# Kernel optimization log

Measured on AMD Instinct MI355X. Metric: run time of the kernel, lower is better.

## Reference

```python
import jax, jax.numpy as jnp
from jax import lax
import numpy as np

B, S, T, R = 64, 50, 50, 2   # batch, n_prev_sents, n_words, n_responses
V, H = 32000, 256            # vocab, hidden (= emb_size)


def gru_scan(xs, h0, Wih, Whh, bih, bhh):
    """Torch-style GRU over xs [T, N, I]; returns (outs [T,N,H], h_last [N,H])."""
    gi_all = jnp.einsum('tni,gi->tng', xs, Wih) + bih  # input gates precomputed
    def step(h, gi):
        gh = h @ Whh.T + bhh
        ir, iz, inn = jnp.split(gi, 3, -1)
        hr, hz, hn = jnp.split(gh, 3, -1)
        r = jax.nn.sigmoid(ir + hr)
        z = jax.nn.sigmoid(iz + hz)
        n = jnp.tanh(inn + r * hn)
        h = (1.0 - z) * n + z * h
        return h, h
    h_last, outs = lax.scan(step, h0, gi_all)
    return outs, h_last


def agent_tables():
    # replicates get_agent_emb: np.random.seed(1), one fresh uniform table per batch
    np.random.seed(1)
    return jnp.asarray(np.stack([np.random.uniform(0, 1, (S + 1, H)) for _ in range(B)]).astype(np.float32))


def setup_inputs() -> dict:
    key = jax.random.key(0)
    ks = jax.random.split(key, 24)
    k = 1.0 / np.sqrt(H)
    u = lambda kk, shape: jax.random.uniform(kk, shape, jnp.float32, -k, k)
    inp = {
        'context': jax.random.randint(ks[0], (B, S, T), 0, V, jnp.int32),
        'response': jax.random.randint(ks[1], (B, R, T), 0, V, jnp.int32),
        'spk_agents': jax.random.randint(ks[2], (B, S), 0, S + 1, jnp.int32),
        'emb_utter': jax.random.normal(ks[3], (V, H), jnp.float32) * 0.1,
        'emb_resp': jax.random.normal(ks[4], (V, H), jnp.float32) * 0.1,
        'utter_Wih': u(ks[5], (3 * H, H)), 'utter_Whh': u(ks[6], (3 * H, H)),
        'utter_bih': u(ks[7], (3 * H,)), 'utter_bhh': u(ks[8], (3 * H,)),
        'ctx_Wih': u(ks[9], (3 * H, 2 * H)), 'ctx_Whh': u(ks[10], (3 * H, H)),
        'ctx_bih': u(ks[11], (3 * H,)), 'ctx_bhh': u(ks[12], (3 * H,)),
        'resp_Wih': u(ks[13], (3 * H, H)), 'resp_Whh': u(ks[14], (3 * H, H)),
        'resp_bih': u(ks[15], (3 * H,)), 'resp_bhh': u(ks[16], (3 * H,)),
        'spk_Wih': u(ks[17], (3 * H, H)), 'spk_Whh': u(ks[18], (3 * H, H)),
        'spk_bih': u(ks[19], (3 * H,)), 'spk_bhh': u(ks[20], (3 * H,)),
    }
    return inp


def forward(context, response, spk_agents, emb_utter, emb_resp,
            utter_Wih, utter_Whh, utter_bih, utter_bhh,
            ctx_Wih, ctx_Whh, ctx_bih, ctx_bhh,
            resp_Wih, resp_Whh, resp_bih, resp_bhh,
            spk_Wih, spk_Whh, spk_bih, spk_bhh):
    # ---- utterance encoder: all B*S utterances batched through one GRU ----
    xu = emb_utter[context.reshape(B * S, T)]                 # [B*S, T, H]
    xu = jnp.transpose(xu, (1, 0, 2))                         # [T, B*S, H]
    _, hu = gru_scan(xu, jnp.zeros((B * S, H), jnp.float32),
                     utter_Wih, utter_Whh, utter_bih, utter_bhh)
    utter_hidden = hu.reshape(B, S, H).transpose(1, 0, 2)     # [S, B, H]

    # ---- agent embeddings (per-batch random tables, gathered by speaker id) ----
    tables = agent_tables()                                   # [B, S+1, H] constant
    agent_emb = jnp.take_along_axis(tables, spk_agents[:, :, None].astype(jnp.int32), axis=1)  # [B,S,H]
    agent_emb = jnp.transpose(agent_emb, (1, 0, 2))           # [S, B, H]

    # ---- context GRU over utterances ----
    ctx_in = jnp.concatenate([utter_hidden, agent_emb], axis=2)  # [S, B, 2H]
    context_output, ctx_h = gru_scan(ctx_in, jnp.zeros((B, H), jnp.float32),
                                     ctx_Wih, ctx_Whh, ctx_bih, ctx_bhh)
    context_hidden = ctx_h[None]                              # [1, B, H]

    # ---- speaker encoder: masked GRU == GRU over each speaker's subsequence ----
    sp_ids = jnp.arange(S + 1)
    active = (spk_agents[:, :, None] == sp_ids[None, None, :])  # [B, S, S+1]
    active_t = jnp.transpose(active, (1, 0, 2))                 # [S, B, S+1]
    gi_all = jnp.einsum('sbh,gh->sbg', context_output, spk_Wih) + spk_bih  # [S, B, 3H]

    def spk_step(h, inputs):
        gi, act = inputs                                        # gi [B,3H], act [B,S+1]
        gh = jnp.einsum('bsh,gh->bsg', h, spk_Whh) + spk_bhh    # [B, S+1, 3H]
        ir, iz, inn = jnp.split(gi[:, None, :], 3, -1)
        hr, hz, hn = jnp.split(gh, 3, -1)
        r = jax.nn.sigmoid(ir + hr)
        z = jax.nn.sigmoid(iz + hz)
        n = jnp.tanh(inn + r * hn)
        h_new = (1.0 - z) * n + z * h
        return jnp.where(act[:, :, None], h_new, h), None

    h_spk, _ = lax.scan(spk_step, jnp.zeros((B, S + 1, H), jnp.float32), (gi_all, active_t))
    present = active.any(axis=1)                               # [B, S+1]
    spk_emb = h_spk * present[:, :, None]                      # rows of absent speakers stay 0
    spk_emb_mask = (present & (sp_ids[None, :] > 0)).astype(jnp.float32)  # [B, S+1]

    # ---- response encoder: all B*R responses batched ----
    xr = emb_resp[response.reshape(B * R, T)]                  # [B*R, T, H]
    xr = jnp.transpose(xr, (1, 0, 2))                          # [T, B*R, H]
    outs, hr_ = gru_scan(xr, jnp.zeros((B * R, H), jnp.float32),
                         resp_Wih, resp_Whh, resp_bih, resp_bhh)
    resp_output = outs.reshape(T, B, R, H).transpose(2, 0, 1, 3)  # [R, T, B, H]
    resp_hidden = hr_.reshape(B, R, H).transpose(1, 0, 2)         # [R, B, H]

    return (context_output, context_hidden, resp_output, resp_hidden, spk_emb, spk_emb_mask)


def reference(context, response, spk_agents, emb_utter, emb_resp,
              utter_Wih, utter_Whh, utter_bih, utter_bhh,
              ctx_Wih, ctx_Whh, ctx_bih, ctx_bhh,
              resp_Wih, resp_Whh, resp_bih, resp_bhh,
              spk_Wih, spk_Whh, spk_bih, spk_bhh):
    return forward(context, response, spk_agents, emb_utter, emb_resp,
                   utter_Wih, utter_Whh, utter_bih, utter_bhh,
                   ctx_Wih, ctx_Whh, ctx_bih, ctx_bhh,
                   resp_Wih, resp_Whh, resp_bih, resp_bhh,
                   spk_Wih, spk_Whh, spk_bih, spk_bhh)
```

## Files before the change

kernel.cpp:

```cpp
#include <hip/hip_runtime.h>
#include <hip/hip_bf16.h>
#include <stdint.h>
#include <stdlib.h>
#include <math.h>

typedef __hip_bfloat16 bf16;
typedef unsigned short ushort;
typedef __attribute__((ext_vector_type(8))) short bhalf8;
typedef __attribute__((ext_vector_type(4))) float f32x4;

#define Bn 64
#define Sn 50
#define Tn 50
#define Hn 256

#define OFF_CTX_OUT   0
#define OFF_CTX_HID   819200
#define OFF_RESP_OUT  835584
#define OFF_RESP_HID  2473984
#define OFF_SPK_EMB   2506752
#define OFF_SPK_MASK  3342336

#define WS_FLAG   0u
#define WS_HU     256u
#define WS_REG    1638912u
#define RG_UTTQ   0u
#define RG_UTTSC  24576000u
#define RG_RESPGI 0u
#define RG_CO     9830400u
#define RG_GIC    13107200u
#define RG_GIS    18022400u
#define RG_TBL    22937600u
#define WS_END    26342912u

__device__ __forceinline__ float b2f_bits(unsigned int b) {
    union { unsigned int u; float f; } c; c.u = b; return c.f;
}
__device__ __forceinline__ float bf2f(ushort v) { return b2f_bits(((unsigned int)v) << 16); }
__device__ __forceinline__ ushort f2bf(float f) {
    union { float f; unsigned int u; } c; c.f = f;
    return (ushort)((c.u + 0x7fffu + ((c.u >> 16) & 1u)) >> 16);
}
__device__ __forceinline__ void gld_lds16(const void* g, void* l) {
    __builtin_amdgcn_global_load_lds(
        (const __attribute__((address_space(1))) void*)g,
        (__attribute__((address_space(3))) void*)l, 16, 0, 0);
}
template<bool BF>
__device__ __forceinline__ bhalf8 ldfrag(const void* __restrict__ p, size_t i) {
    if (BF) {
        return *(const bhalf8*)((const ushort*)p + i);
    } else {
        const float* q = (const float*)p + i;
        float4 a = *(const float4*)q;
        float4 b = *(const float4*)(q + 4);
        bhalf8 r;
        r[0] = (short)f2bf(a.x); r[1] = (short)f2bf(a.y);
        r[2] = (short)f2bf(a.z); r[3] = (short)f2bf(a.w);
        r[4] = (short)f2bf(b.x); r[5] = (short)f2bf(b.y);
        r[6] = (short)f2bf(b.z); r[7] = (short)f2bf(b.w);
        return r;
    }
}
template<bool BF>
__device__ __forceinline__ float ldw(const void* __restrict__ p, int i) {
    return BF ? bf2f(((const ushort*)p)[i]) : ((const float*)p)[i];
}
template<bool BF>
__device__ __forceinline__ void stout(void* __restrict__ out, size_t i, float v) {
    if (BF) ((ushort*)out)[i] = f2bf(v);
    else    ((float*)out)[i] = v;
}
__device__ __forceinline__ float fsigm(float x) {
    return __builtin_amdgcn_rcpf(1.f + __expf(-x));
}
__device__ __forceinline__ float ftanh(float x) {
    float e = __expf(-2.f * x);
    return (1.f - e) * __builtin_amdgcn_rcpf(1.f + e);
}

__global__ void sniff_kernel(const void* __restrict__ w, int* __restrict__ flag) {
    const unsigned int* p = (const unsigned int*)w;
    int tid = threadIdx.x;
    bool big = false;
// ... 230 lines not shown
    const int* __restrict__ rsp_tok, const void* __restrict__ emb_r,
    const void* __restrict__ rWih, const void* __restrict__ rbih,
    ushort* __restrict__ RG, float* bhs)
{
    const int tid = threadIdx.x;
    const int w = tid >> 6, l = tid & 63, quad = l >> 4, c = l & 15;

    for (int i = tid; i < 768; i += 512) bhs[i] = ldw<BF>(rbih, i);

    bhalf8 wf[3][2][8];
    #pragma unroll
    for (int g = 0; g < 3; ++g)
        #pragma unroll
        for (int ctl = 0; ctl < 2; ++ctl) {
            const int gcol = g * 256 + 32 * w + 16 * ctl + c;
            #pragma unroll
            for (int tk = 0; tk < 8; ++tk)
                wf[g][ctl][tk] = ldfrag<BF>(rWih, (size_t)gcol * 256 + 32 * tk + 8 * quad);
        }
    __syncthreads();

    const int inst = bid * 16 + c;
    const int tok  = rsp_tok[inst];

    f32x4 acc[3][2];
    #pragma unroll
    for (int g = 0; g < 3; ++g)
        #pragma unroll
        for (int ctl = 0; ctl < 2; ++ctl) {
            float b = bhs[g * 256 + 32 * w + 16 * ctl + c];
            acc[g][ctl] = (f32x4){b, b, b, b};
        }
    #pragma unroll
    for (int tk = 0; tk < 8; ++tk) {
        bhalf8 a = ldfrag<BF>(emb_r, (size_t)tok * 256 + 32 * tk + 8 * quad);
        #pragma unroll
        for (int g = 0; g < 3; ++g)
            #pragma unroll
            for (int ctl = 0; ctl < 2; ++ctl)
                acc[g][ctl] = __builtin_amdgcn_mfma_f32_16x16x32_bf16(
                    a, wf[g][ctl][tk], acc[g][ctl], 0, 0, 0);
    }
    #pragma unroll
    for (int g = 0; g < 3; ++g)
        #pragma unroll
        for (int ctl = 0; ctl < 2; ++ctl)
            #pragma unroll
            for (int r = 0; r < 4; ++r)
                RG[(size_t)(bid * 16 + 4 * quad + r) * 768
                   + g * 256 + 32 * w + 16 * ctl + c] = f2bf(acc[g][ctl][r]);
}

template<bool BF>
__device__ void rec_resp_body(
    int bid,
    const ushort* __restrict__ RG,
    const void* __restrict__ rWhh, const void* __restrict__ rbhh,
    void* __restrict__ outp,
    ushort (*gx)[16][776], ushort (*hb)[16][264])
{
    const int n0 = bid * 16;
    const int tid = threadIdx.x;
    const int w = tid >> 6, l = tid & 63, quad = l >> 4, c = l & 15;

    for (int i = tid; i < 16 * 264; i += 512) (&hb[0][0][0])[i] = 0;

    float breg[3][2];
    #pragma unroll
    for (int g = 0; g < 3; ++g)
        #pragma unroll
        for (int ctl = 0; ctl < 2; ++ctl)
            breg[g][ctl] = ldw<BF>(rbhh, g * 256 + 32 * w + 16 * ctl + c);

    bhalf8 wf[3][2][8];
    #pragma unroll
    for (int g = 0; g < 3; ++g)
        #pragma unroll
        for (int ctl = 0; ctl < 2; ++ctl) {
            const int gcol = g * 256 + 32 * w + 16 * ctl + c;
            #pragma unroll
            for (int tk = 0; tk < 8; ++tk)
                wf[g][ctl][tk] = ldfrag<BF>(rWhh, (size_t)gcol * 256 + 32 * tk + 8 * quad);
        }

    float st[2][4];
    #pragma unroll
    for (int ctl = 0; ctl < 2; ++ctl)
        #pragma unroll
        for (int r = 0; r < 4; ++r) st[ctl][r] = 0.f;

    #pragma unroll
    for (int k = 0; k < 2; ++k) {
        const int m = 2 * w + k;
        const ushort* src = RG + (size_t)((n0 + m) * Tn + 0) * 768;
        if (l < 48) {
            gld_lds16(src + l * 8,       &gx[0][m][0]);
            gld_lds16(src + 384 + l * 8, &gx[0][m][384]);
        }
    }
    __syncthreads();

    int p = 0;
    for (int t = 0; t < Tn; ++t) {
        if (t < Tn - 1) {
            #pragma unroll
            for (int k = 0; k < 2; ++k) {
                const int m = 2 * w + k;
                const ushort* src = RG + (size_t)((n0 + m) * Tn + t + 1) * 768;
                if (l < 48) {
                    gld_lds16(src + l * 8,       &gx[p ^ 1][m][0]);
                    gld_lds16(src + 384 + l * 8, &gx[p ^ 1][m][384]);
                }
            }
// ... 15 lines not shown
        f32x4 acc[3][2];
        #pragma unroll
        for (int g = 0; g < 3; ++g)
            #pragma unroll
            for (int ctl = 0; ctl < 2; ++ctl) {
                float b = breg[g][ctl];
                acc[g][ctl] = (f32x4){b, b, b, b};
            }
        #pragma unroll
        for (int tk = 0; tk < 8; ++tk) {
            bhalf8 a = *(const bhalf8*)(&hb[p][c][32 * tk + 8 * quad]);
            #pragma unroll
            for (int g = 0; g < 3; ++g)
                #pragma unroll
                for (int ctl = 0; ctl < 2; ++ctl)
                    acc[g][ctl] = __builtin_amdgcn_mfma_f32_16x16x32_bf16(
                        a, wf[g][ctl][tk], acc[g][ctl], 0, 0, 0);
        }

        #pragma unroll
        for (int ctl = 0; ctl < 2; ++ctl) {
            const int u = 32 * w + 16 * ctl + c;
            #pragma unroll
            for (int r = 0; r < 4; ++r) {
                const int m = 4 * quad + r;
                float gr = bf2f(gx[p][m][u]);
                float gz = bf2f(gx[p][m][256 + u]);
                float gn = bf2f(gx[p][m][512 + u]);
                float rr = fsigm(gr + acc[0][ctl][r]);
                float zz = fsigm(gz + acc[1][ctl][r]);
                float nn = ftanh(gn + rr * acc[2][ctl][r]);
                float h  = (1.f - zz) * nn + zz * st[ctl][r];
                st[ctl][r] = h;
                hb[p ^ 1][m][u] = f2bf(h);
            }
        }
        __syncthreads();
        p ^= 1;
    }

    #pragma unroll
    for (int ctl = 0; ctl < 2; ++ctl) {
        const int u = 32 * w + 16 * ctl + c;
        #pragma unroll
        for (int r = 0; r < 4; ++r) {
            const int n = n0 + 4 * quad + r, bb = n >> 1, ri = n & 1;
            stout<BF>(outp, OFF_RESP_OUT
                      + (size_t)((ri * Tn + (Tn - 1)) * Bn + bb) * Hn + u, st[ctl][r]);
            stout<BF>(outp, OFF_RESP_HID + (size_t)(ri * Bn + bb) * Hn + u, st[ctl][r]);
        }
    }
}

template<bool BF>
__device__ void gi_ctx_body(
    int bid,
    const ushort* __restrict__ H_u, const ushort* __restrict__ tblbf,
    const int* __restrict__ spk_agents,
    const void* __restrict__ Wih, const void* __restrict__ bih,
    ushort* __restrict__ GIc, float* bhs)
{
    const int tid = threadIdx.x;
    const int w = tid >> 6, l = tid & 63, quad = l >> 4, c = l & 15;

    for (int i = tid; i < 768; i += 512) bhs[i] = ldw<BF>(bih, i);
    __syncthreads();

    const int m0 = bid * 16;
    const int m  = m0 + c, s = m >> 6, b = m & 63;
    const int a  = spk_agents[b * Sn + s];
    const ushort* arow0 = H_u   + (size_t)(b * Sn + s) * Hn;
    const ushort* arow1 = tblbf + (size_t)(b * 51 + a) * Hn;

    f32x4 acc[3][2];
    #pragma unroll
    for (int g = 0; g < 3; ++g)
        #pragma unroll
        for (int ctl = 0; ctl < 2; ++ctl) {
            float bb = bhs[g * 256 + 32 * w + 16 * ctl + c];
            acc[g][ctl] = (f32x4){bb, bb, bb, bb};
        }

    for (int half = 0; half < 2; ++half) {
        const ushort* ar = half ? arow1 : arow0;
        bhalf8 af[8];
        #pragma unroll
        for (int tk = 0; tk < 8; ++tk)
            af[tk] = *(const bhalf8*)(ar + 32 * tk + 8 * quad);
        #pragma unroll
        for (int g = 0; g < 3; ++g) {
            bhalf8 wf[2][8];
            #pragma unroll
            for (int ctl = 0; ctl < 2; ++ctl) {
                const int gcol = g * 256 + 32 * w + 16 * ctl + c;
                #pragma unroll
                for (int tk = 0; tk < 8; ++tk)
                    wf[ctl][tk] = ldfrag<BF>(Wih,
                        (size_t)gcol * 512 + half * 256 + 32 * tk + 8 * quad);
            }
            #pragma unroll
            for (int tk = 0; tk < 8; ++tk)
                #pragma unroll
                for (int ctl = 0; ctl < 2; ++ctl)
                    acc[g][ctl] = __builtin_amdgcn_mfma_f32_16x16x32_bf16(
                        af[tk], wf[ctl][tk], acc[g][ctl], 0, 0, 0);
        }
    }

    #pragma unroll
    for (int g = 0; g < 3; ++g)
        #pragma unroll
        for (int ctl = 0; ctl < 2; ++ctl)
            #pragma unroll
            for (int r = 0; r < 4; ++r)
                GIc[(size_t)(m0 + 4 * quad + r) * 768
                    + g * 256 + 32 * w + 16 * ctl + c] = f2bf(acc[g][ctl][r]);
}

__global__ __launch_bounds__(512, 1) void gates2_kernel(
    const int* rsp_tok, const void* emb_r, const void* rWih, const void* rbih,
    ushort* RG,
    const ushort* H_u, const ushort* tblbf, const int* spk_agents,
    const void* cWih, const void* cbih, ushort* GIc, const int* flag)
{
    __shared__ float bhs[768];
    if (blockIdx.x < 400) {
        if (*flag) respgi_body<true >(blockIdx.x, rsp_tok, emb_r, rWih, rbih, RG, bhs);
        else       respgi_body<false>(blockIdx.x, rsp_tok, emb_r, rWih, rbih, RG, bhs);
    } else {
        const int bid = blockIdx.x - 400;
        if (*flag) gi_ctx_body<true >(bid, H_u, tblbf, spk_agents, cWih, cbih, GIc, bhs);
        else       gi_ctx_body<false>(bid, H_u, tblbf, spk_agents, cWih, cbih, GIc, bhs);
    }
}

template<bool BF>
__device__ void ctx_rec_body(
    int bid,
    const ushort* __restrict__ GIc,
    const void* __restrict__ Whh, const void* __restrict__ bhh,
    float* __restrict__ CO, void* __restrict__ outp,
    ushort (*gx)[16][776], ushort (*hb)[16][264])
{
    const int n0 = bid * 16;
    const int tid = threadIdx.x;
    const int w = tid >> 6, l = tid & 63, quad = l >> 4, c = l & 15;

    for (int i = tid; i < 16 * 264; i += 512) (&hb[0][0][0])[i] = 0;

    float breg[3][2];
    #pragma unroll
    for (int g = 0; g < 3; ++g)
        #pragma unroll
        for (int ctl = 0; ctl < 2; ++ctl)
            breg[g][ctl] = ldw<BF>(bhh, g * 256 + 32 * w + 16 * ctl + c);

    bhalf8 wf[3][2][8];
    #pragma unroll
    for (int g = 0; g < 3; ++g)
        #pragma unroll
        for (int ctl = 0; ctl < 2; ++ctl) {
            const int gcol = g * 256 + 32 * w + 16 * ctl + c;
            #pragma unroll
            for (int tk = 0; tk < 8; ++tk)
                wf[g][ctl][tk] = ldfrag<BF>(Whh, (size_t)gcol * 256 + 32 * tk + 8 * quad);
        }

    float st[2][4];
    #pragma unroll
    for (int ctl = 0; ctl < 2; ++ctl)
        #pragma unroll
        for (int r = 0; r < 4; ++r) st[ctl][r] = 0.f;

    #pragma unroll
    for (int k = 0; k < 2; ++k) {
        const int m = 2 * w + k;
        const ushort* src = GIc + (size_t)(0 * Bn + n0 + m) * 768;
        if (l < 48) {
            gld_lds16(src + l * 8,       &gx[0][m][0]);
            gld_lds16(src + 384 + l * 8, &gx[0][m][384]);
        }
    }
    __syncthreads();

    int p = 0;
    for (int t = 0; t < Sn; ++t) {
        if (t < Sn - 1) {
            #pragma unroll
            for (int k = 0; k < 2; ++k) {
                const int m = 2 * w + k;
                const ushort* src = GIc + (size_t)((t + 1) * Bn + n0 + m) * 768;
                if (l < 48) {
                    gld_lds16(src + l * 8,       &gx[p ^ 1][m][0]);
                    gld_lds16(src + 384 + l * 8, &gx[p ^ 1][m][384]);
                }
            }
        }
        if (t > 0) {
            #pragma unroll
            for (int ctl = 0; ctl < 2; ++ctl) {
                const int u = 32 * w + 16 * ctl + c;
                #pragma unroll
                for (int r = 0; r < 4; ++r) {
                    const size_t gri = (size_t)((t - 1) * Bn + n0 + 4 * quad + r);
                    CO[gri * Hn + u] = st[ctl][r];
                    stout<BF>(outp, OFF_CTX_OUT + gri * Hn + u, st[ctl][r]);
                }
            }
        }

        f32x4 acc[3][2];
        #pragma unroll
        for (int g = 0; g < 3; ++g)
            #pragma unroll
            for (int ctl = 0; ctl < 2; ++ctl) {
                float b = breg[g][ctl];
                acc[g][ctl] = (f32x4){b, b, b, b};
            }
        #pragma unroll
        for (int tk = 0; tk < 8; ++tk) {
            bhalf8 a = *(const bhalf8*)(&hb[p][c][32 * tk + 8 * quad]);
            #pragma unroll
            for (int g = 0; g < 3; ++g)
                #pragma unroll
                for (int ctl = 0; ctl < 2; ++ctl)
                    acc[g][ctl] = __builtin_amdgcn_mfma_f32_16x16x32_bf16(
                        a, wf[g][ctl][tk], acc[g][ctl], 0, 0, 0);
        }

        #pragma unroll
        for (int ctl = 0; ctl < 2; ++ctl) {
            const int u = 32 * w + 16 * ctl + c;
            #pragma unroll
            for (int r = 0; r < 4; ++r) {
                const int m = 4 * quad + r;
                float gr = bf2f(gx[p][m][u]);
                float gz = bf2f(gx[p][m][256 + u]);
                float gn = bf2f(gx[p][m][512 + u]);
                float rr = fsigm(gr + acc[0][ctl][r]);
                float zz = fsigm(gz + acc[1][ctl][r]);
                float nn = ftanh(gn + rr * acc[2][ctl][r]);
                float h  = (1.f - zz) * nn + zz * st[ctl][r];
                st[ctl][r] = h;
                hb[p ^ 1][m][u] = f2bf(h);
            }
        }
        __syncthreads();
        p ^= 1;
    }

    #pragma unroll
    for (int ctl = 0; ctl < 2; ++ctl) {
        const int u = 32 * w + 16 * ctl + c;
        #pragma unroll
        for (int r = 0; r < 4; ++r) {
            const int m = 4 * quad + r;
            const size_t gri = (size_t)((Sn - 1) * Bn + n0 + m);
            CO[gri * Hn + u] = st[ctl][r];
            stout<BF>(outp, OFF_CTX_OUT + gri * Hn + u, st[ctl][r]);
            stout<BF>(outp, OFF_CTX_HID + (size_t)(n0 + m) * Hn + u, st[ctl][r]);
        }
    }
}

__global__ __launch_bounds__(512, 1) void rec2_kernel(
    const ushort* GIc, const void* cWhh, const void* cbhh, float* CO,
    const ushort* RG, const void* rWhh, const void* rbhh,
    void* outp, const int* flag)
{
    __shared__ __align__(16) ushort gx[2][16][776];
    __shared__ __align__(16) ushort hb[2][16][264];
    if (blockIdx.x < 4) {
        if (*flag) ctx_rec_body<true >(blockIdx.x, GIc, cWhh, cbhh, CO, outp, gx, hb);
        else       ctx_rec_body<false>(blockIdx.x, GIc, cWhh, cbhh, CO, outp, gx, hb);
    } else {
        const int bid = blockIdx.x - 4;
        if (*flag) rec_resp_body<true >(bid, RG, rWhh, rbhh, outp, gx, hb);
        else       rec_resp_body<false>(bid, RG, rWhh, rbhh, outp, gx, hb);
    }
}

template<bool BF>
__device__ void gi_spk_body(
    const float* __restrict__ CO,
    const void* __restrict__ Wih, const void* __restrict__ bih,
    ushort* __restrict__ GIs, float* bhs)
{
    const int tid = threadIdx.x;
    const int w = tid >> 6, l = tid & 63, quad = l >> 4, c = l & 15;

    for (int i = tid; i < 768; i += 512) bhs[i] = ldw<BF>(bih, i);

    bhalf8 wf[3][2][8];
    #pragma unroll
    for (int g = 0; g < 3; ++g)
        #pragma unroll
        for (int ctl = 0; ctl < 2; ++ctl) {
            const int gcol = g * 256 + 32 * w + 16 * ctl + c;
            #pragma unroll
            for (int tk = 0; tk < 8; ++tk)
                wf[g][ctl][tk] = ldfrag<BF>(Wih, (size_t)gcol * 256 + 32 * tk + 8 * quad);
        }
    __syncthreads();

    f32x4 acc[3][2];
    #pragma unroll
    for (int g = 0; g < 3; ++g)
        #pragma unroll
        for (int ctl = 0; ctl < 2; ++ctl) {
            float b = bhs[g * 256 + 32 * w + 16 * ctl + c];
            acc[g][ctl] = (f32x4){b, b, b, b};
        }
    #pragma unroll
    for (int tk = 0; tk < 8; ++tk) {
        bhalf8 a = ldfrag<false>(CO, (size_t)(blockIdx.x * 16 + c) * 256 + 32 * tk + 8 * quad);
        #pragma unroll
        for (int g = 0; g < 3; ++g)
            #pragma unroll
            for (int ctl = 0; ctl < 2; ++ctl)
                acc[g][ctl] = __builtin_amdgcn_mfma_f32_16x16x32_bf16(
                    a, wf[g][ctl][tk], acc[g][ctl], 0, 0, 0);
    }
    #pragma unroll
    for (int g = 0; g < 3; ++g)
        #pragma unroll
        for (int ctl = 0; ctl < 2; ++ctl)
            #pragma unroll
            for (int r = 0; r < 4; ++r)
                GIs[(size_t)(blockIdx.x * 16 + 4 * quad + r) * 768
                    + g * 256 + 32 * w + 16 * ctl + c] = f2bf(acc[g][ctl][r]);
}

__global__ __launch_bounds__(512, 1) void gi_spk_kernel(
    const float* CO, const void* Wih, const void* bih, ushort* GIs, const int* flag)
{
    __shared__ float bhs[768];
    if (*flag) gi_spk_body<true >(CO, Wih, bih, GIs, bhs);
    else       gi_spk_body<false>(CO, Wih, bih, GIs, bhs);
}

#define SSTR 264
template<bool BF>
__device__ void spk_rec_body(
    const ushort* __restrict__ GIs,
    const void* __restrict__ Whh, const void* __restrict__ bhh,
    const int* __restrict__ spk_agents,
    void* __restrict__ outp,
    ushort* S , ushort (*gx)[4][776], int* pres , float* bhs)
{
    const int b0 = blockIdx.x * 4;
    const int tid = threadIdx.x;
    const int w = tid >> 6, l = tid & 63, quad = l >> 4, c = l & 15;

    for (int i = tid; i < 768; i += 512) bhs[i] = ldw<BF>(bhh, i);
    for (int i = tid; i < 4 * 51 * SSTR; i += 512) S[i] = 0;
    for (int i = tid; i < 4 * 51; i += 512) pres[i] = 0;

    bhalf8 wf[3][2][8];
    #pragma unroll
    for (int g = 0; g < 3; ++g)
        #pragma unroll
        for (int ctl = 0; ctl < 2; ++ctl) {
            const int gcol = g * 256 + 32 * w + 16 * ctl + c;
            #pragma unroll
            for (int tk = 0; tk < 8; ++tk)
                wf[g][ctl][tk] = ldfrag<BF>(Whh, (size_t)gcol * 256 + 32 * tk + 8 * quad);
        }

    {
        const int row = w >> 1, ch = w & 1;
        const ushort* src = GIs + (size_t)(0 * Bn + b0 + row) * 768 + ch * 384;
        if (l < 48) gld_lds16(src + l * 8, &gx[0][row][ch * 384]);
    }
    __syncthreads();

    int p = 0;
    for (int t = 0; t < Sn; ++t) {
        const int va = (c < 4) ? spk_agents[(b0 + c) * Sn + t] : 0;
        const int mb = (c < 4) ? c : 0;

        if (t < Sn - 1) {
            const int row = w >> 1, ch = w & 1;
            const ushort* src = GIs + (size_t)((t + 1) * Bn + b0 + row) * 768 + ch * 384;
            if (l < 48) gld_lds16(src + l * 8, &gx[p ^ 1][row][ch * 384]);
        }

        f32x4 acc[3][2];
        #pragma unroll
        for (int g = 0; g < 3; ++g)
            #pragma unroll
            for (int ctl = 0; ctl < 2; ++ctl) {
                float b = bhs[g * 256 + 32 * w + 16 * ctl + c];
                acc[g][ctl] = (f32x4){b, b, b, b};
            }
        const ushort* srow = &S[(mb * 51 + va) * SSTR];
        #pragma unroll
        for (int tk = 0; tk < 8; ++tk) {
            bhalf8 a = *(const bhalf8*)(srow + 32 * tk + 8 * quad);
            #pragma unroll
            for (int g = 0; g < 3; ++g)
                #pragma unroll
                for (int ctl = 0; ctl < 2; ++ctl)
                    acc[g][ctl] = __builtin_amdgcn_mfma_f32_16x16x32_bf16(
                        a, wf[g][ctl][tk], acc[g][ctl], 0, 0, 0);
        }
        __syncthreads();

        if (quad == 0) {
            int vv[4];
            #pragma unroll
            for (int r = 0; r < 4; ++r) vv[r] = spk_agents[(b0 + r) * Sn + t];
            #pragma unroll
            for (int ctl = 0; ctl < 2; ++ctl) {
                const int u = 32 * w + 16 * ctl + c;
                #pragma unroll
                for (int r = 0; r < 4; ++r) {
                    ushort* sp = &S[(r * 51 + vv[r]) * SSTR + u];
                    float gr = bf2f(gx[p][r][u]);
                    float gz = bf2f(gx[p][r][256 + u]);
                    float gn = bf2f(gx[p][r][512 + u]);
                    float hprev = bf2f(*sp);
                    float rr = fsigm(gr + acc[0][ctl][r]);
                    float zz = fsigm(gz + acc[1][ctl][r]);
                    float nn = ftanh(gn + rr * acc[2][ctl][r]);
                    float h  = (1.f - zz) * nn + zz * hprev;
                    *sp = f2bf(h);
                }
            }
        }
        if (tid < 4) pres[tid * 51 + spk_agents[(b0 + tid) * Sn + t]] = 1;
        __syncthreads();
        p ^= 1;
    }
    __syncthreads();

    for (int idx = tid; idx < 4 * 51 * 256; idx += 512) {
        const int mb2 = idx / (51 * 256);
        const int rem = idx - mb2 * (51 * 256);
        const int v = rem >> 8, u = rem & 255;
        float val = bf2f(S[(mb2 * 51 + v) * SSTR + u]);
        stout<BF>(outp, OFF_SPK_EMB + (size_t)((b0 + mb2) * 51 + v) * Hn + u, val);
    }
    for (int idx = tid; idx < 4 * 51; idx += 512) {
        const int mb2 = idx / 51, v = idx - mb2 * 51;
        stout<BF>(outp, OFF_SPK_MASK + (size_t)((b0 + mb2) * 51 + v),
                  (pres[mb2 * 51 + v] && v > 0) ? 1.f : 0.f);
    }
}

__global__ __launch_bounds__(512, 1) void spk_rec_kernel(
    const ushort* GIs, const void* Whh, const void* bhh,
    const int* spk_agents, void* outp, const int* flag)
{
    __shared__ __align__(16) ushort S[4 * 51 * SSTR];
    __shared__ __align__(16) ushort gx[2][4][776];
    __shared__ int    pres[4 * 51];
    __shared__ float  bhs[768];
    if (*flag) spk_rec_body<true >(GIs, Whh, bhh, spk_agents, outp, S, gx, pres, bhs);
    else       spk_rec_body<false>(GIs, Whh, bhh, spk_agents, outp, S, gx, pres, bhs);
}

namespace {
inline uint16_t host_f2bf(float f) {
    union { float f; uint32_t u; } c; c.f = f;
    return (uint16_t)((c.u + 0x7fffu + ((c.u >> 16) & 1u)) >> 16);
}
struct MT19937 {
    uint32_t mt[624]; int mti;
    void seed(uint32_t s) {
        mt[0] = s;
        for (int i = 1; i < 624; ++i)
            mt[i] = 1812433253u * (mt[i - 1] ^ (mt[i - 1] >> 30)) + (uint32_t)i;
        mti = 624;
    }
    uint32_t next() {
        if (mti >= 624) {
            for (int i = 0; i < 624; ++i) {
                uint32_t y = (mt[i] & 0x80000000u) | (mt[(i + 1) % 624] & 0x7fffffffu);
                mt[i] = mt[(i + 397) % 624] ^ (y >> 1) ^ ((y & 1u) ? 0x9908b0dfu : 0u);
            }
            mti = 0;
        }
        uint32_t y = mt[mti++];
        y ^= y >> 11; y ^= (y << 7) & 0x9d2c5680u; y ^= (y << 15) & 0xefc60000u; y ^= y >> 18;
        return y;
    }
    double rd() {
        uint32_t a = next() >> 5, b = next() >> 6;
        return (a * 67108864.0 + b) / 9007199254740992.0;
    }
};

uint16_t* get_host_tables() {
    static uint16_t* p = [] {
        void* q = nullptr;
        if (hipHostMalloc(&q, 835584 * sizeof(uint16_t), hipHostMallocDefault) != hipSuccess)
            q = malloc(835584 * sizeof(uint16_t));
        uint16_t* h = (uint16_t*)q;
        MT19937 g; g.seed(1u);
        for (int i = 0; i < 835584; ++i)
            h[i] = host_f2bf((float)g.rd());
        return h;
    }();
    return p;
}
}

extern "C" void kernel_launch(void* const* d_in, const int* in_sizes, int n_in,
                              void* d_out, int out_size, void* d_ws, size_t ws_size,
                              hipStream_t stream)
{
    const int* ctx_tok    = (const int*)d_in[0];
    const int* rsp_tok    = (const int*)d_in[1];
    const int* spk_agents = (const int*)d_in[2];
    const void* emb_u = d_in[3];
    const void* emb_r = d_in[4];
    const void* uWih = d_in[5],  *uWhh = d_in[6],  *ubih = d_in[7],  *ubhh = d_in[8];
    const void* cWih = d_in[9],  *cWhh = d_in[10], *cbih = d_in[11], *cbhh = d_in[12];
    const void* rWih = d_in[13], *rWhh = d_in[14], *rbih = d_in[15], *rbhh = d_in[16];
    const void* sWih = d_in[17], *sWhh = d_in[18], *sbih = d_in[19], *sbhh = d_in[20];
    (void)in_sizes; (void)n_in; (void)out_size; (void)ws_size;

    char* ws  = (char*)d_ws;
    char* reg = ws + WS_REG;
    int*      flag = (int*)(ws + WS_FLAG);
    ushort*   H_u  = (ushort*)(ws + WS_HU);
    char*     UQ   = (char*)(reg + RG_UTTQ);
    float*    USC  = (float*)(reg + RG_UTTSC);
    ushort*   RG   = (ushort*)(reg + RG_RESPGI);
    float*    CO   = (float*)(reg + RG_CO);
    ushort*   GIc  = (ushort*)(reg + RG_GIC);
    ushort*   GIs  = (ushort*)(reg + RG_GIS);
    ushort*   tbl  = (ushort*)(reg + RG_TBL);
    void*     out  = d_out;

    sniff_kernel<<<1, 64, 0, stream>>>(uWih, flag);

    vocab_utt_kernel<<<250, 512, 0, stream>>>(emb_u, uWih, ubih, UQ, USC, flag);
    rec_utt_kernel<<<200, 512, 0, stream>>>(ctx_tok, UQ, USC, uWhh, ubhh, H_u, flag);

    hipMemcpyAsync(tbl, get_host_tables(), 835584 * sizeof(uint16_t),
                   hipMemcpyHostToDevice, stream);

    gates2_kernel<<<600, 512, 0, stream>>>(rsp_tok, emb_r, rWih, rbih, RG,
                                           H_u, tbl, spk_agents, cWih, cbih, GIc, flag);

    rec2_kernel<<<12, 512, 0, stream>>>(GIc, cWhh, cbhh, CO,
                                        RG, rWhh, rbhh, out, flag);

    gi_spk_kernel<<<200, 512, 0, stream>>>(CO, sWih, sbih, GIs, flag);
    spk_rec_kernel<<<16, 512, 0, stream>>>(GIs, sWhh, sbhh, spk_agents, out, flag);
}
```

Before: 1.236 ms.

## Fuse context GRU recurrence, speaker input gates and speaker recurrence into one kernel

Replaces the context recurrence, the speaker input-gate GEMM and the speaker recurrence kernels with a single kernel. Each block now handles 4 batches through the context GRU and feeds each step's hidden state directly into the speaker GRU, computing the speaker input gates per step instead of precomputing them. This removes two launches, the CO and GIs global round trips and a grid-wide dependency. In exchange, weights are reloaded from global/cache every step rather than held in registers, context parallelism falls to 16 blocks of 4 rows, and the speaker work is now serialized behind the context recurrence inside each block.

```diff
diff --git a/kernel.cpp b/kernel.cpp
--- a/kernel.cpp
+++ b/kernel.cpp
@@ -27,9 +27,7 @@
 #define RG_UTTQ   0u
 #define RG_UTTSC  24576000u
 #define RG_RESPGI 0u
-#define RG_CO     9830400u
 #define RG_GIC    13107200u
-#define RG_GIS    18022400u
 #define RG_TBL    22937600u
 #define WS_END    26342912u
 
@@ -366,13 +364,97 @@
 }
 
 template<bool BF>
+__device__ void gi_ctx_body(
+    int bid,
+    const ushort* __restrict__ H_u, const ushort* __restrict__ tblbf,
+    const int* __restrict__ spk_agents,
+    const void* __restrict__ Wih, const void* __restrict__ bih,
+    ushort* __restrict__ GIc, float* bhs)
+{
+    const int tid = threadIdx.x;
+    const int w = tid >> 6, l = tid & 63, quad = l >> 4, c = l & 15;
+
+    for (int i = tid; i < 768; i += 512) bhs[i] = ldw<BF>(bih, i);
+    __syncthreads();
+
+    const int m0 = bid * 16;
+    const int m  = m0 + c, s = m >> 6, b = m & 63;
+    const int a  = spk_agents[b * Sn + s];
+    const ushort* arow0 = H_u   + (size_t)(b * Sn + s) * Hn;
+    const ushort* arow1 = tblbf + (size_t)(b * 51 + a) * Hn;
+
+    f32x4 acc[3][2];
+    #pragma unroll
+    for (int g = 0; g < 3; ++g)
+        #pragma unroll
+        for (int ctl = 0; ctl < 2; ++ctl) {
+            float bb = bhs[g * 256 + 32 * w + 16 * ctl + c];
+            acc[g][ctl] = (f32x4){bb, bb, bb, bb};
+        }
+
+    for (int half = 0; half < 2; ++half) {
+        const ushort* ar = half ? arow1 : arow0;
+        bhalf8 af[8];
+        #pragma unroll
+        for (int tk = 0; tk < 8; ++tk)
+            af[tk] = *(const bhalf8*)(ar + 32 * tk + 8 * quad);
+        #pragma unroll
+        for (int g = 0; g < 3; ++g) {
+            bhalf8 wfl[2][8];
+            #pragma unroll
+            for (int ctl = 0; ctl < 2; ++ctl) {
+                const int gcol = g * 256 + 32 * w + 16 * ctl + c;
+                #pragma unroll
+                for (int tk = 0; tk < 8; ++tk)
+                    wfl[ctl][tk] = ldfrag<BF>(Wih,
+                        (size_t)gcol * 512 + half * 256 + 32 * tk + 8 * quad);
+            }
+            #pragma unroll
+            for (int tk = 0; tk < 8; ++tk)
+                #pragma unroll
+                for (int ctl = 0; ctl < 2; ++ctl)
+                    acc[g][ctl] = __builtin_amdgcn_mfma_f32_16x16x32_bf16(
+                        af[tk], wfl[ctl][tk], acc[g][ctl], 0, 0, 0);
+        }
+    }
+
+    #pragma unroll
+    for (int g = 0; g < 3; ++g)
+        #pragma unroll
+        for (int ctl = 0; ctl < 2; ++ctl)
+            #pragma unroll
+            for (int r = 0; r < 4; ++r)
+                GIc[(size_t)(m0 + 4 * quad + r) * 768
+                    + g * 256 + 32 * w + 16 * ctl + c] = f2bf(acc[g][ctl][r]);
+}
+
+__global__ __launch_bounds__(512, 1) void gates2_kernel(
+    const int* rsp_tok, const void* emb_r, const void* rWih, const void* rbih,
+    ushort* RG,
+    const ushort* H_u, const ushort* tblbf, const int* spk_agents,
+    const void* cWih, const void* cbih, ushort* GIc, const int* flag)
+{
+    __shared__ float bhs[768];
+    if (blockIdx.x < 400) {
+        if (*flag) respgi_body<true >(blockIdx.x, rsp_tok, emb_r, rWih, rbih, RG, bhs);
+        else       respgi_body<false>(blockIdx.x, rsp_tok, emb_r, rWih, rbih, RG, bhs);
+    } else {
+        const int bid = blockIdx.x - 400;
+        if (*flag) gi_ctx_body<true >(bid, H_u, tblbf, spk_agents, cWih, cbih, GIc, bhs);
+        else       gi_ctx_body<false>(bid, H_u, tblbf, spk_agents, cWih, cbih, GIc, bhs);
+    }
+}
+
+template<bool BF>
 __device__ void rec_resp_body(
     int bid,
     const ushort* __restrict__ RG,
     const void* __restrict__ rWhh, const void* __restrict__ rbhh,
-    void* __restrict__ outp,
-    ushort (*gx)[16][776], ushort (*hb)[16][264])
-{
+    void* __restrict__ outp, char* smem)
+{
+    ushort (*gx)[16][776] = (ushort(*)[16][776])(smem);
+    ushort (*hb)[16][264] = (ushort(*)[16][264])(smem + 49664);
+
     const int n0 = bid * 16;
     const int tid = threadIdx.x;
     const int w = tid >> 6, l = tid & 63, quad = l >> 4, c = l & 15;
@@ -494,119 +576,37 @@
     }
 }
 
+#define SSTR 264
 template<bool BF>
-__device__ void gi_ctx_body(
+__device__ void mega_body(
     int bid,
-    const ushort* __restrict__ H_u, const ushort* __restrict__ tblbf,
+    const ushort* __restrict__ GIc,
+    const void* __restrict__ cWhh, const void* __restrict__ cbhh,
+    const void* __restrict__ sWih, const void* __restrict__ sbih,
+    const void* __restrict__ sWhh, const void* __restrict__ sbhh,
     const int* __restrict__ spk_agents,
-    const void* __restrict__ Wih, const void* __restrict__ bih,
-    ushort* __restrict__ GIc, float* bhs)
-{
+    void* __restrict__ outp, char* smem)
+{
+    ushort* S             = (ushort*)smem;
+    ushort (*hc)[16][264] = (ushort(*)[16][264])(smem + 107712);
+    ushort (*gic)[4][776] = (ushort(*)[4][776])(smem + 124608);
+    int*    pres          = (int*)(smem + 137024);
+    float*  cbh           = (float*)(smem + 137840);
+    float*  sbi           = cbh + 768;
+    float*  sbh           = sbi + 768;
+
+    const int b0 = bid * 4;
     const int tid = threadIdx.x;
     const int w = tid >> 6, l = tid & 63, quad = l >> 4, c = l & 15;
 
-    for (int i = tid; i < 768; i += 512) bhs[i] = ldw<BF>(bih, i);
-    __syncthreads();
-
-    const int m0 = bid * 16;
-    const int m  = m0 + c, s = m >> 6, b = m & 63;
-    const int a  = spk_agents[b * Sn + s];
-    const ushort* arow0 = H_u   + (size_t)(b * Sn + s) * Hn;
-    const ushort* arow1 = tblbf + (size_t)(b * 51 + a) * Hn;
-
-    f32x4 acc[3][2];
-    #pragma unroll
-    for (int g = 0; g < 3; ++g)
-        #pragma unroll
-        for (int ctl = 0; ctl < 2; ++ctl) {
-            float bb = bhs[g * 256 + 32 * w + 16 * ctl + c];
-            acc[g][ctl] = (f32x4){bb, bb, bb, bb};
-        }
-
-    for (int half = 0; half < 2; ++half) {
-        const ushort* ar = half ? arow1 : arow0;
-        bhalf8 af[8];
-        #pragma unroll
-        for (int tk = 0; tk < 8; ++tk)
-            af[tk] = *(const bhalf8*)(ar + 32 * tk + 8 * quad);
-        #pragma unroll
-        for (int g = 0; g < 3; ++g) {
-            bhalf8 wf[2][8];
-            #pragma unroll
-            for (int ctl = 0; ctl < 2; ++ctl) {
-                const int gcol = g * 256 + 32 * w + 16 * ctl + c;
-                #pragma unroll
-                for (int tk = 0; tk < 8; ++tk)
-                    wf[ctl][tk] = ldfrag<BF>(Wih,
-                        (size_t)gcol * 512 + half * 256 + 32 * tk + 8 * quad);
-            }
-            #pragma unroll
-            for (int tk = 0; tk < 8; ++tk)
-                #pragma unroll
-                for (int ctl = 0; ctl < 2; ++ctl)
-                    acc[g][ctl] = __builtin_amdgcn_mfma_f32_16x16x32_bf16(
-                        af[tk], wf[ctl][tk], acc[g][ctl], 0, 0, 0);
-        }
-    }
-
-    #pragma unroll
-    for (int g = 0; g < 3; ++g)
-        #pragma unroll
-        for (int ctl = 0; ctl < 2; ++ctl)
-            #pragma unroll
-            for (int r = 0; r < 4; ++r)
-                GIc[(size_t)(m0 + 4 * quad + r) * 768
-                    + g * 256 + 32 * w + 16 * ctl + c] = f2bf(acc[g][ctl][r]);
-}
-
-__global__ __launch_bounds__(512, 1) void gates2_kernel(
-    const int* rsp_tok, const void* emb_r, const void* rWih, const void* rbih,
-    ushort* RG,
-    const ushort* H_u, const ushort* tblbf, const int* spk_agents,
-    const void* cWih, const void* cbih, ushort* GIc, const int* flag)
-{
-    __shared__ float bhs[768];
-    if (blockIdx.x < 400) {
-        if (*flag) respgi_body<true >(blockIdx.x, rsp_tok, emb_r, rWih, rbih, RG, bhs);
-        else       respgi_body<false>(blockIdx.x, rsp_tok, emb_r, rWih, rbih, RG, bhs);
-    } else {
-        const int bid = blockIdx.x - 400;
-        if (*flag) gi_ctx_body<true >(bid, H_u, tblbf, spk_agents, cWih, cbih, GIc, bhs);
-        else       gi_ctx_body<false>(bid, H_u, tblbf, spk_agents, cWih, cbih, GIc, bhs);
-    }
-}
-
-template<bool BF>
-__device__ void ctx_rec_body(
-    int bid,
-    const ushort* __restrict__ GIc,
-    const void* __restrict__ Whh, const void* __restrict__ bhh,
-    float* __restrict__ CO, void* __restrict__ outp,
-    ushort (*gx)[16][776], ushort (*hb)[16][264])
-{
-    const int n0 = bid * 16;
-    const int tid = threadIdx.x;
-    const int w = tid >> 6, l = tid & 63, quad = l >> 4, c = l & 15;
-
-    for (int i = tid; i < 16 * 264; i += 512) (&hb[0][0][0])[i] = 0;
-
-    float breg[3][2];
-    #pragma unroll
-    for (int g = 0; g < 3; ++g)
-        #pragma unroll
-        for (int ctl = 0; ctl < 2; ++ctl)
-            breg[g][ctl] = ldw<BF>(bhh, g * 256 + 32 * w + 16 * ctl + c);
-
-    bhalf8 wf[3][2][8];
-    #pragma unroll
-    for (int g = 0; g < 3; ++g)
-        #pragma unroll
-        for (int ctl = 0; ctl < 2; ++ctl) {
-            const int gcol = g * 256 + 32 * w + 16 * ctl + c;
-            #pragma unroll
-            for (int tk = 0; tk < 8; ++tk)
-                wf[g][ctl][tk] = ldfrag<BF>(Whh, (size_t)gcol * 256 + 32 * tk + 8 * quad);
-        }
+    for (int i = tid; i < 4 * 51 * SSTR; i += 512) S[i] = 0;
+    for (int i = tid; i < 2 * 16 * 264; i += 512) (&hc[0][0][0])[i] = 0;
+    for (int i = tid; i < 4 * 51; i += 512) pres[i] = 0;
+    for (int i = tid; i < 768; i += 512) {
+        cbh[i] = ldw<BF>(cbhh, i);
+        sbi[i] = ldw<BF>(sbih, i);
+        sbh[i] = ldw<BF>(sbhh, i);
+    }
 
     float st[2][4];
     #pragma unroll
@@ -614,238 +614,125 @@
         #pragma unroll
         for (int r = 0; r < 4; ++r) st[ctl][r] = 0.f;
 
-    #pragma unroll
-    for (int k = 0; k < 2; ++k) {
-        const int m = 2 * w + k;
-        const ushort* src = GIc + (size_t)(0 * Bn + n0 + m) * 768;
-        if (l < 48) {
-            gld_lds16(src + l * 8,       &gx[0][m][0]);
-            gld_lds16(src + 384 + l * 8, &gx[0][m][384]);
-        }
+    {
+        const int row = w >> 1, ch = w & 1;
+        const ushort* src = GIc + (size_t)(0 * Bn + b0 + row) * 768 + ch * 384;
+        if (l < 48) gld_lds16(src + l * 8, &gic[0][row][ch * 384]);
     }
     __syncthreads();
 
     int p = 0;
     for (int t = 0; t < Sn; ++t) {
         if (t < Sn - 1) {
-            #pragma unroll
-            for (int k = 0; k < 2; ++k) {
-                const int m = 2 * w + k;
-                const ushort* src = GIc + (size_t)((t + 1) * Bn + n0 + m) * 768;
-                if (l < 48) {
-                    gld_lds16(src + l * 8,       &gx[p ^ 1][m][0]);
-                    gld_lds16(src + 384 + l * 8, &gx[p ^ 1][m][384]);
+            const int row = w >> 1, ch = w & 1;
+            const ushort* src = GIc + (size_t)((t + 1) * Bn + b0 + row) * 768 + ch * 384;
+            if (l < 48) gld_lds16(src + l * 8, &gic[p ^ 1][row][ch * 384]);
+        }
+
+        bhalf8 areg[8];
+        #pragma unroll
+        for (int tk = 0; tk < 8; ++tk)
+            areg[tk] = *(const bhalf8*)(&hc[p][c][32 * tk + 8 * quad]);
+        f32x4 accc[3][2];
+        #pragma unroll
+        for (int g = 0; g < 3; ++g)
+            #pragma unroll
+            for (int ctl = 0; ctl < 2; ++ctl) {
+                float b = cbh[g * 256 + 32 * w + 16 * ctl + c];
+                accc[g][ctl] = (f32x4){b, b, b, b};
+            }
+        #pragma unroll
+        for (int g = 0; g < 3; ++g)
+            #pragma unroll
+            for (int ctl = 0; ctl < 2; ++ctl) {
+                const int gcol = g * 256 + 32 * w + 16 * ctl + c;
+                bhalf8 wt[8];
+                #pragma unroll
+                for (int tk = 0; tk < 8; ++tk)
+                    wt[tk] = ldfrag<BF>(cWhh, (size_t)gcol * 256 + 32 * tk + 8 * quad);
+                #pragma unroll
+                for (int tk = 0; tk < 8; ++tk)
+                    accc[g][ctl] = __builtin_amdgcn_mfma_f32_16x16x32_bf16(
+                        areg[tk], wt[tk], accc[g][ctl], 0, 0, 0);
+            }
+        if (quad == 0) {
+            #pragma unroll
+            for (int ctl = 0; ctl < 2; ++ctl) {
+                const int u = 32 * w + 16 * ctl + c;
+                #pragma unroll
+                for (int r = 0; r < 4; ++r) {
+                    float gr = bf2f(gic[p][r][u]);
+                    float gz = bf2f(gic[p][r][256 + u]);
+                    float gn = bf2f(gic[p][r][512 + u]);
+                    float rr = fsigm(gr + accc[0][ctl][r]);
+                    float zz = fsigm(gz + accc[1][ctl][r]);
+                    float nn = ftanh(gn + rr * accc[2][ctl][r]);
+                    float h  = (1.f - zz) * nn + zz * st[ctl][r];
+                    st[ctl][r] = h;
+                    hc[p ^ 1][r][u] = f2bf(h);
+                    const size_t gri = (size_t)(t * Bn + b0 + r);
+                    stout<BF>(outp, OFF_CTX_OUT + gri * Hn + u, h);
+                    if (t == Sn - 1)
+                        stout<BF>(outp, OFF_CTX_HID + (size_t)(b0 + r) * Hn + u, h);
                 }
             }
         }
-        if (t > 0) {
-            #pragma unroll
-            for (int ctl = 0; ctl < 2; ++ctl) {
-                const int u = 32 * w + 16 * ctl + c;
-                #pragma unroll
-                for (int r = 0; r < 4; ++r) {
-                    const size_t gri = (size_t)((t - 1) * Bn + n0 + 4 * quad + r);
-                    CO[gri * Hn + u] = st[ctl][r];
-                    stout<BF>(outp, OFF_CTX_OUT + gri * Hn + u, st[ctl][r]);
-                }
-            }
-        }
-
-        f32x4 acc[3][2];
-        #pragma unroll
-        for (int g = 0; g < 3; ++g)
-            #pragma unroll
-            for (int ctl = 0; ctl < 2; ++ctl) {
-                float b = breg[g][ctl];
-                acc[g][ctl] = (f32x4){b, b, b, b};
-            }
-        #pragma unroll
-        for (int tk = 0; tk < 8; ++tk) {
-            bhalf8 a = *(const bhalf8*)(&hb[p][c][32 * tk + 8 * quad]);
-            #pragma unroll
-            for (int g = 0; g < 3; ++g)
-                #pragma unroll
-                for (int ctl = 0; ctl < 2; ++ctl)
-                    acc[g][ctl] = __builtin_amdgcn_mfma_f32_16x16x32_bf16(
-                        a, wf[g][ctl][tk], acc[g][ctl], 0, 0, 0);
-        }
-
-        #pragma unroll
-        for (int ctl = 0; ctl < 2; ++ctl) {
-            const int u = 32 * w + 16 * ctl + c;
-            #pragma unroll
-            for (int r = 0; r < 4; ++r) {
-                const int m = 4 * quad + r;
-                float gr = bf2f(gx[p][m][u]);
-                float gz = bf2f(gx[p][m][256 + u]);
-                float gn = bf2f(gx[p][m][512 + u]);
-                float rr = fsigm(gr + acc[0][ctl][r]);
-                float zz = fsigm(gz + acc[1][ctl][r]);
-                float nn = ftanh(gn + rr * acc[2][ctl][r]);
-                float h  = (1.f - zz) * nn + zz * st[ctl][r];
-                st[ctl][r] = h;
-                hb[p ^ 1][m][u] = f2bf(h);
-            }
-        }
         __syncthreads();
-        p ^= 1;
-    }
-
-    #pragma unroll
-    for (int ctl = 0; ctl < 2; ++ctl) {
-        const int u = 32 * w + 16 * ctl + c;
-        #pragma unroll
-        for (int r = 0; r < 4; ++r) {
-            const int m = 4 * quad + r;
-            const size_t gri = (size_t)((Sn - 1) * Bn + n0 + m);
-            CO[gri * Hn + u] = st[ctl][r];
-            stout<BF>(outp, OFF_CTX_OUT + gri * Hn + u, st[ctl][r]);
-            stout<BF>(outp, OFF_CTX_HID + (size_t)(n0 + m) * Hn + u, st[ctl][r]);
-        }
-    }
-}
-
-__global__ __launch_bounds__(512, 1) void rec2_kernel(
-    const ushort* GIc, const void* cWhh, const void* cbhh, float* CO,
-    const ushort* RG, const void* rWhh, const void* rbhh,
-    void* outp, const int* flag)
-{
-    __shared__ __align__(16) ushort gx[2][16][776];
-    __shared__ __align__(16) ushort hb[2][16][264];
-    if (blockIdx.x < 4) {
-        if (*flag) ctx_rec_body<true >(blockIdx.x, GIc, cWhh, cbhh, CO, outp, gx, hb);
-        else       ctx_rec_body<false>(blockIdx.x, GIc, cWhh, cbhh, CO, outp, gx, hb);
-    } else {
-        const int bid = blockIdx.x - 4;
-        if (*flag) rec_resp_body<true >(bid, RG, rWhh, rbhh, outp, gx, hb);
-        else       rec_resp_body<false>(bid, RG, rWhh, rbhh, outp, gx, hb);
-    }
-}
-
-template<bool BF>
-__device__ void gi_spk_body(
-    const float* __restrict__ CO,
-    const void* __restrict__ Wih, const void* __restrict__ bih,
-    ushort* __restrict__ GIs, float* bhs)
-{
-    const int tid = threadIdx.x;
-    const int w = tid >> 6, l = tid & 63, quad = l >> 4, c = l & 15;
-
-    for (int i = tid; i < 768; i += 512) bhs[i] = ldw<BF>(bih, i);
-
-    bhalf8 wf[3][2][8];
-    #pragma unroll
-    for (int g = 0; g < 3; ++g)
-        #pragma unroll
-        for (int ctl = 0; ctl < 2; ++ctl) {
-            const int gcol = g * 256 + 32 * w + 16 * ctl + c;
-            #pragma unroll
-            for (int tk = 0; tk < 8; ++tk)
-                wf[g][ctl][tk] = ldfrag<BF>(Wih, (size_t)gcol * 256 + 32 * tk + 8 * quad);
-        }
-    __syncthreads();
-
-    f32x4 acc[3][2];
-    #pragma unroll
-    for (int g = 0; g < 3; ++g)
-        #pragma unroll
-        for (int ctl = 0; ctl < 2; ++ctl) {
-            float b = bhs[g * 256 + 32 * w + 16 * ctl + c];
-            acc[g][ctl] = (f32x4){b, b, b, b};
-        }
-    #pragma unroll
-    for (int tk = 0; tk < 8; ++tk) {
-        bhalf8 a = ldfrag<false>(CO, (size_t)(blockIdx.x * 16 + c) * 256 + 32 * tk + 8 * quad);
-        #pragma unroll
-        for (int g = 0; g < 3; ++g)
-            #pragma unroll
-            for (int ctl = 0; ctl < 2; ++ctl)
-                acc[g][ctl] = __builtin_amdgcn_mfma_f32_16x16x32_bf16(
-                    a, wf[g][ctl][tk], acc[g][ctl], 0, 0, 0);
-    }
-    #pragma unroll
-    for (int g = 0; g < 3; ++g)
-        #pragma unroll
-        for (int ctl = 0; ctl < 2; ++ctl)
-            #pragma unroll
-            for (int r = 0; r < 4; ++r)
-                GIs[(size_t)(blockIdx.x * 16 + 4 * quad + r) * 768
-                    + g * 256 + 32 * w + 16 * ctl + c] = f2bf(acc[g][ctl][r]);
-}
-
-__global__ __launch_bounds__(512, 1) void gi_spk_kernel(
-    const float* CO, const void* Wih, const void* bih, ushort* GIs, const int* flag)
-{
-    __shared__ float bhs[768];
-    if (*flag) gi_spk_body<true >(CO, Wih, bih, GIs, bhs);
-    else       gi_spk_body<false>(CO, Wih, bih, GIs, bhs);
-}
-
-#define SSTR 264
-template<bool BF>
-__device__ void spk_rec_body(
-    const ushort* __restrict__ GIs,
-    const void* __restrict__ Whh, const void* __restrict__ bhh,
-    const int* __restrict__ spk_agents,
-    void* __restrict__ outp,
-    ushort* S , ushort (*gx)[4][776], int* pres , float* bhs)
-{
-    const int b0 = blockIdx.x * 4;
-    const int tid = threadIdx.x;
-    const int w = tid >> 6, l = tid & 63, quad = l >> 4, c = l & 15;
-
-    for (int i = tid; i < 768; i += 512) bhs[i] = ldw<BF>(bhh, i);
-    for (int i = tid; i < 4 * 51 * SSTR; i += 512) S[i] = 0;
-    for (int i = tid; i < 4 * 51; i += 512) pres[i] = 0;
-
-    bhalf8 wf[3][2][8];
-    #pragma unroll
-    for (int g = 0; g < 3; ++g)
-        #pragma unroll
-        for (int ctl = 0; ctl < 2; ++ctl) {
-            const int gcol = g * 256 + 32 * w + 16 * ctl + c;
-            #pragma unroll
-            for (int tk = 0; tk < 8; ++tk)
-                wf[g][ctl][tk] = ldfrag<BF>(Whh, (size_t)gcol * 256 + 32 * tk + 8 * quad);
-        }
-
-    {
-        const int row = w >> 1, ch = w & 1;
-        const ushort* src = GIs + (size_t)(0 * Bn + b0 + row) * 768 + ch * 384;
-        if (l < 48) gld_lds16(src + l * 8, &gx[0][row][ch * 384]);
-    }
-    __syncthreads();
-
-    int p = 0;
-    for (int t = 0; t < Sn; ++t) {
+
+        #pragma unroll
+        for (int tk = 0; tk < 8; ++tk)
+            areg[tk] = *(const bhalf8*)(&hc[p ^ 1][c][32 * tk + 8 * quad]);
+        f32x4 accs[3][2];
+        #pragma unroll
+        for (int g = 0; g < 3; ++g)
+            #pragma unroll
+            for (int ctl = 0; ctl < 2; ++ctl) {
+                float b = sbi[g * 256 + 32 * w + 16 * ctl + c];
+                accs[g][ctl] = (f32x4){b, b, b, b};
+            }
+        #pragma unroll
+        for (int g = 0; g < 3; ++g)
+            #pragma unroll
+            for (int ctl = 0; ctl < 2; ++ctl) {
+                const int gcol = g * 256 + 32 * w + 16 * ctl + c;
+                bhalf8 wt[8];
+                #pragma unroll
+                for (int tk = 0; tk < 8; ++tk)
+                    wt[tk] = ldfrag<BF>(sWih, (size_t)gcol * 256 + 32 * tk + 8 * quad);
+                #pragma unroll
+                for (int tk = 0; tk < 8; ++tk)
+                    accs[g][ctl] = __builtin_amdgcn_mfma_f32_16x16x32_bf16(
+                        areg[tk], wt[tk], accs[g][ctl], 0, 0, 0);
+            }
+
         const int va = (c < 4) ? spk_agents[(b0 + c) * Sn + t] : 0;
         const int mb = (c < 4) ? c : 0;
-
-        if (t < Sn - 1) {
-            const int row = w >> 1, ch = w & 1;
-            const ushort* src = GIs + (size_t)((t + 1) * Bn + b0 + row) * 768 + ch * 384;
-            if (l < 48) gld_lds16(src + l * 8, &gx[p ^ 1][row][ch * 384]);
-        }
-
-        f32x4 acc[3][2];
-        #pragma unroll
-        for (int g = 0; g < 3; ++g)
-            #pragma unroll
-            for (int ctl = 0; ctl < 2; ++ctl) {
-                float b = bhs[g * 256 + 32 * w + 16 * ctl + c];
-                acc[g][ctl] = (f32x4){b, b, b, b};
-            }
         const ushort* srow = &S[(mb * 51 + va) * SSTR];
         #pragma unroll
-        for (int tk = 0; tk < 8; ++tk) {
-            bhalf8 a = *(const bhalf8*)(srow + 32 * tk + 8 * quad);
-            #pragma unroll
-            for (int g = 0; g < 3; ++g)
-                #pragma unroll
-                for (int ctl = 0; ctl < 2; ++ctl)
-                    acc[g][ctl] = __builtin_amdgcn_mfma_f32_16x16x32_bf16(
-                        a, wf[g][ctl][tk], acc[g][ctl], 0, 0, 0);
-        }
+        for (int tk = 0; tk < 8; ++tk)
+            areg[tk] = *(const bhalf8*)(srow + 32 * tk + 8 * quad);
+        f32x4 acch[3][2];
+        #pragma unroll
+        for (int g = 0; g < 3; ++g)
+            #pragma unroll
+            for (int ctl = 0; ctl < 2; ++ctl) {
+                float b = sbh[g * 256 + 32 * w + 16 * ctl + c];
+                acch[g][ctl] = (f32x4){b, b, b, b};
+            }
+        #pragma unroll
+        for (int g = 0; g < 3; ++g)
+            #pragma unroll
+            for (int ctl = 0; ctl < 2; ++ctl) {
+                const int gcol = g * 256 + 32 * w + 16 * ctl + c;
+                bhalf8 wt[8];
+                #pragma unroll
+                for (int tk = 0; tk < 8; ++tk)
+                    wt[tk] = ldfrag<BF>(sWhh, (size_t)gcol * 256 + 32 * tk + 8 * quad);
+                #pragma unroll
+                for (int tk = 0; tk < 8; ++tk)
+                    acch[g][ctl] = __builtin_amdgcn_mfma_f32_16x16x32_bf16(
+                        areg[tk], wt[tk], acch[g][ctl], 0, 0, 0);
+            }
         __syncthreads();
 
         if (quad == 0) {
@@ -858,13 +745,10 @@
                 #pragma unroll
                 for (int r = 0; r < 4; ++r) {
                     ushort* sp = &S[(r * 51 + vv[r]) * SSTR + u];
-                    float gr = bf2f(gx[p][r][u]);
-                    float gz = bf2f(gx[p][r][256 + u]);
-                    float gn = bf2f(gx[p][r][512 + u]);
                     float hprev = bf2f(*sp);
-                    float rr = fsigm(gr + acc[0][ctl][r]);
-                    float zz = fsigm(gz + acc[1][ctl][r]);
-                    float nn = ftanh(gn + rr * acc[2][ctl][r]);
+                    float rr = fsigm(accs[0][ctl][r] + acch[0][ctl][r]);
+                    float zz = fsigm(accs[1][ctl][r] + acch[1][ctl][r]);
+                    float nn = ftanh(accs[2][ctl][r] + rr * acch[2][ctl][r]);
                     float h  = (1.f - zz) * nn + zz * hprev;
                     *sp = f2bf(h);
                 }
@@ -874,7 +758,6 @@
         __syncthreads();
         p ^= 1;
     }
-    __syncthreads();
 
     for (int idx = tid; idx < 4 * 51 * 256; idx += 512) {
         const int mb2 = idx / (51 * 256);
@@ -890,16 +773,24 @@
     }
 }
 
-__global__ __launch_bounds__(512, 1) void spk_rec_kernel(
-    const ushort* GIs, const void* Whh, const void* bhh,
-    const int* spk_agents, void* outp, const int* flag)
-{
-    __shared__ __align__(16) ushort S[4 * 51 * SSTR];
-    __shared__ __align__(16) ushort gx[2][4][776];
-    __shared__ int    pres[4 * 51];
-    __shared__ float  bhs[768];
-    if (*flag) spk_rec_body<true >(GIs, Whh, bhh, spk_agents, outp, S, gx, pres, bhs);
-    else       spk_rec_body<false>(GIs, Whh, bhh, spk_agents, outp, S, gx, pres, bhs);
+__global__ __launch_bounds__(512, 1) void tail_kernel(
+    const ushort* GIc, const void* cWhh, const void* cbhh,
+    const void* sWih, const void* sbih, const void* sWhh, const void* sbhh,
+    const int* spk_agents,
+    const ushort* RG, const void* rWhh, const void* rbhh,
+    void* outp, const int* flag)
+{
+    __shared__ __align__(16) char smem[147056];
+    if (blockIdx.x < 16) {
+        if (*flag) mega_body<true >(blockIdx.x, GIc, cWhh, cbhh, sWih, sbih,
+                                    sWhh, sbhh, spk_agents, outp, smem);
+        else       mega_body<false>(blockIdx.x, GIc, cWhh, cbhh, sWih, sbih,
+                                    sWhh, sbhh, spk_agents, outp, smem);
+    } else {
+        const int bid = blockIdx.x - 16;
+        if (*flag) rec_resp_body<true >(bid, RG, rWhh, rbhh, outp, smem);
+        else       rec_resp_body<false>(bid, RG, rWhh, rbhh, outp, smem);
+    }
 }
 
 namespace {
@@ -970,9 +861,7 @@
     char*     UQ   = (char*)(reg + RG_UTTQ);
     float*    USC  = (float*)(reg + RG_UTTSC);
     ushort*   RG   = (ushort*)(reg + RG_RESPGI);
-    float*    CO   = (float*)(reg + RG_CO);
     ushort*   GIc  = (ushort*)(reg + RG_GIC);
-    ushort*   GIs  = (ushort*)(reg + RG_GIS);
     ushort*   tbl  = (ushort*)(reg + RG_TBL);
     void*     out  = d_out;
 
@@ -987,9 +876,6 @@
     gates2_kernel<<<600, 512, 0, stream>>>(rsp_tok, emb_r, rWih, rbih, RG,
                                            H_u, tbl, spk_agents, cWih, cbih, GIc, flag);
 
-    rec2_kernel<<<12, 512, 0, stream>>>(GIc, cWhh, cbhh, CO,
-                                        RG, rWhh, rbhh, out, flag);
-
-    gi_spk_kernel<<<200, 512, 0, stream>>>(CO, sWih, sbih, GIs, flag);
-    spk_rec_kernel<<<16, 512, 0, stream>>>(GIs, sWhh, sbhh, spk_agents, out, flag);
-}
+    tail_kernel<<<24, 512, 0, stream>>>(GIc, cWhh, cbhh, sWih, sbih, sWhh, sbhh,
+                                        spk_agents, RG, rWhh, rbhh, out, flag);
+}
```

Result: slower. 2.187 ms (+76.9%).
